# Kernel optimization log

Hardware: AMD Instinct MI355X
Metric: run time of the kernel (lower is better)

The kernel has to match this reference:

```python
import jax, jax.numpy as jnp
import numpy as np

N = 144      # Lx*Ly lattice sites (12x12)
NH = 256     # GRU hidden units
K = 2        # local Hilbert dim (occupied/empty)
LOG_EPS = 1e-10


def _gru_step(h, x, kernel, rec_kernel, bias):
    # Keras GRU cell, reset_after=True, gate order (z, r, h)
    gx = x @ kernel + bias[0]        # [B, 3*NH]
    gh = h @ rec_kernel + bias[1]    # [B, 3*NH]
    xz, xr, xh = jnp.split(gx, 3, axis=-1)
    hz, hr, hn = jnp.split(gh, 3, axis=-1)
    z = jax.nn.sigmoid(xz + hz)
    r = jax.nn.sigmoid(xr + hr)
    hh = jnp.tanh(xh + r * hn)
    return z * h + (1.0 - z) * hh


def setup_inputs() -> dict:
    key = jax.random.key(0)
    k1, k2, k3 = jax.random.split(key, 3)
    glorot = lambda k, shape: jax.random.uniform(
        k, shape, jnp.float32,
        -jnp.sqrt(6.0 / (shape[0] + shape[1])),
        jnp.sqrt(6.0 / (shape[0] + shape[1])))
    return {
        "kernel": glorot(k1, (K, 3 * NH)),
        "rec_kernel": glorot(k2, (NH, 3 * NH)),
        "bias": jnp.zeros((2, 3 * NH), jnp.float32),
        "dense_w": glorot(k3, (NH, K)),
        "dense_b": jnp.zeros((K,), jnp.float32),
        "nsamples": 1024,
    }


def reference(kernel, rec_kernel, bias, dense_w, dense_b, nsamples):
    h0 = jnp.zeros((nsamples, NH), jnp.float32)
    x0 = jnp.zeros((nsamples, K), jnp.float32)   # 0.0 * one_hot(0)
    logP0 = jnp.zeros((nsamples,), jnp.float32)
    keys = jax.random.split(jax.random.key(42), N)

    def step(carry, step_key):
        h, x, logP = carry
        h = _gru_step(h, x, kernel, rec_kernel, bias)
        probs = jax.nn.softmax(h @ dense_w + dense_b)          # [B, K]
        log_probs = jnp.log(LOG_EPS + probs)                   # matches tf.math.log(1e-10+p)
        s = jax.random.categorical(step_key, log_probs)        # [B] int
        x_new = jax.nn.one_hot(s, K, dtype=jnp.float32)
        logP = logP + jnp.take_along_axis(log_probs, s[:, None], axis=1)[:, 0]
        return (h, x_new, logP), s

    (_, _, logP), samples = jax.lax.scan(step, (h0, x0, logP0), keys)
    samples = samples.T  # [nsamples, N]
    return samples, logP
```

## Files before the change

kernel.cpp:

```cpp
#include <hip/hip_runtime.h>
#include <stdint.h>

#define N_SITES 144
#define NHID    256
#define NSAMP   1024
#define MB      4
#define TPB     768
#define PARTITIONABLE 1

__device__ __forceinline__ uint32_t rotl32(uint32_t v, uint32_t r) {
    return (v << r) | (v >> (32u - r));
}

__device__ __forceinline__ void threefry(uint32_t k0, uint32_t k1,
                                         uint32_t x0, uint32_t x1,
                                         uint32_t& o0, uint32_t& o1) {
    uint32_t ks0 = k0, ks1 = k1, ks2 = k0 ^ k1 ^ 0x1BD11BDAu;
    x0 += ks0; x1 += ks1;
#define RG4(a,b,c,d) \
    x0 += x1; x1 = rotl32(x1,a); x1 ^= x0; \
    x0 += x1; x1 = rotl32(x1,b); x1 ^= x0; \
    x0 += x1; x1 = rotl32(x1,c); x1 ^= x0; \
    x0 += x1; x1 = rotl32(x1,d); x1 ^= x0;
    RG4(13,15,26,6)  x0 += ks1; x1 += ks2 + 1u;
    RG4(17,29,16,24) x0 += ks2; x1 += ks0 + 2u;
    RG4(13,15,26,6)  x0 += ks0; x1 += ks1 + 3u;
    RG4(17,29,16,24) x0 += ks1; x1 += ks2 + 4u;
    RG4(13,15,26,6)  x0 += ks2; x1 += ks0 + 5u;
#undef RG4
    o0 = x0; o1 = x1;
}

__device__ __forceinline__ float gumbel_from_bits(uint32_t bits) {
#pragma clang fp contract(off)
    const float TINY = 1.17549435e-38f;
    uint32_t fb = (bits >> 9) | 0x3f800000u;
    float u = __uint_as_float(fb) - 1.0f;
    u = u * (1.0f - TINY) + TINY;
    u = fmaxf(TINY, u);
    return -logf(-logf(u));
}

__global__ __launch_bounds__(TPB, 1)
void rnn_sample_kernel(const float* __restrict__ kern,
                       const float* __restrict__ rec,
                       const float* __restrict__ bias,
                       const float* __restrict__ dw,
                       const float* __restrict__ db,
                       float* __restrict__ out)
{
    const int t    = threadIdx.x;
    const int blk  = blockIdx.x;
    const int b0   = blk * MB;
    const int wv   = t >> 6;
    const int lane = t & 63;

    __shared__ float4   hs4[NHID];
    __shared__ float    pacc[MB][TPB];
    __shared__ uint32_t keyA[N_SITES], keyB[N_SITES];
    __shared__ float    wred[4][8];
    __shared__ int      sPrev[MB];
    __shared__ float    lgP[MB];

    float kz0 = 0.f, kr0 = 0.f, kn0 = 0.f, kz1 = 0.f, kr1 = 0.f, kn1 = 0.f;
    float b0z = 0.f, b0r = 0.f, b0n = 0.f, b1z = 0.f, b1r = 0.f, b1n = 0.f;
    float dwa = 0.f, dwb = 0.f, dba = 0.f, dbb = 0.f;
    if (t < NHID) {
        const int c0 = t, c1 = t + 256, c2 = t + 512;
        kz0 = kern[c0];       kr0 = kern[c1];       kn0 = kern[c2];
        kz1 = kern[768 + c0]; kr1 = kern[768 + c1]; kn1 = kern[768 + c2];
        b0z = bias[c0];       b0r = bias[c1];       b0n = bias[c2];
        b1z = bias[768 + c0]; b1r = bias[768 + c1]; b1n = bias[768 + c2];
        dwa = dw[2 * t];      dwb = dw[2 * t + 1];
        dba = db[0];          dbb = db[1];
        hs4[t] = make_float4(0.f, 0.f, 0.f, 0.f);
    }
    if (t < MB) { sPrev[t] = -1; lgP[t] = 0.f; }
    if (t < N_SITES) {
        uint32_t o0, o1;
        threefry(0u, 42u, 0u, (uint32_t)t, o0, o1);
        keyA[t] = o0; keyB[t] = o1;
    }
    __syncthreads();

    for (int n = 0; n < N_SITES; ++n) {
        float a0 = 0.f, a1 = 0.f, a2 = 0.f, a3 = 0.f;
        {
            const float* rp = rec + t;
#pragma unroll 8
            for (int k = 0; k < NHID; ++k) {
                float4 h4 = hs4[k];
                float w  = rp[0];
                rp += 768;
                a0 = fmaf(h4.x, w, a0);
                a1 = fmaf(h4.y, w, a1);
                a2 = fmaf(h4.z, w, a2);
                a3 = fmaf(h4.w, w, a3);
            }
        }
        pacc[0][t] = a0; pacc[1][t] = a1; pacc[2][t] = a2; pacc[3][t] = a3;
        __syncthreads();

        float hnew[MB];
        if (t < NHID) {
            float4 ho = hs4[t];
            float hold[MB] = { ho.x, ho.y, ho.z, ho.w };
            {
#pragma clang fp contract(off)
#pragma unroll
                for (int m = 0; m < MB; ++m) {
                    const int sp = sPrev[m];
                    float xz = (sp == 0) ? kz0 : ((sp == 1) ? kz1 : 0.f);
                    float xr = (sp == 0) ? kr0 : ((sp == 1) ? kr1 : 0.f);
                    float xh = (sp == 0) ? kn0 : ((sp == 1) ? kn1 : 0.f);
                    xz = xz + b0z;  xr = xr + b0r;  xh = xh + b0n;
                    const float hz = pacc[m][t]       + b1z;
                    const float hr = pacc[m][t + 256] + b1r;
                    const float hn = pacc[m][t + 512] + b1n;
                    const float z = 1.0f / (1.0f + expf(-(xz + hz)));
                    const float r = 1.0f / (1.0f + expf(-(xr + hr)));
                    const float rhn = r * hn;
                    const float hh = tanhf(xh + rhn);
                    hnew[m] = z * hold[m] + (1.0f - z) * hh;
                }
            }
            hs4[t] = make_float4(hnew[0], hnew[1], hnew[2], hnew[3]);

#pragma unroll
            for (int m = 0; m < MB; ++m) {
                float va = hnew[m] * dwa;
                float vb = hnew[m] * dwb;
#pragma unroll
                for (int off = 32; off > 0; off >>= 1) {
                    va += __shfl_xor(va, off, 64);
                    vb += __shfl_xor(vb, off, 64);
                }
                if (lane == 0) { wred[wv][2 * m] = va; wred[wv][2 * m + 1] = vb; }
            }
        }
        __syncthreads();

        if (t < MB) {
            const int m = t;
            float l0 = wred[0][2 * m] + wred[1][2 * m] + wred[2][2 * m] + wred[3][2 * m];
            float l1 = wred[0][2 * m + 1] + wred[1][2 * m + 1] + wred[2][2 * m + 1] + wred[3][2 * m + 1];
            uint32_t o0a, o1a, o0b, o1b;
            const uint32_t fbase = 2u * (uint32_t)(b0 + m);
            threefry(keyA[n], keyB[n], 0u, fbase,      o0a, o1a);
            threefry(keyA[n], keyB[n], 0u, fbase + 1u, o0b, o1b);
            const float g0 = gumbel_from_bits(o0a ^ o1a);
            const float g1 = gumbel_from_bits(o0b ^ o1b);
            {
#pragma clang fp contract(off)
                l0 = l0 + dba;
                l1 = l1 + dbb;
                const float mx = fmaxf(l0, l1);
                const float e0 = expf(l0 - mx), e1 = expf(l1 - mx);
                const float den = e0 + e1;
                const float lp0 = logf(1e-10f + e0 / den);
                const float lp1 = logf(1e-10f + e1 / den);
                const float v0 = g0 + lp0;
                const float v1 = g1 + lp1;
                const int s = (v1 > v0) ? 1 : 0;
                sPrev[m] = s;
                lgP[m] = lgP[m] + (s ? lp1 : lp0);
                out[(size_t)(b0 + m) * N_SITES + n] = (float)s;
            }
        }
        __syncthreads();
    }

    if (t < MB) out[(size_t)NSAMP * N_SITES + (b0 + t)] = lgP[t];
}

extern "C" void kernel_launch(void* const* d_in, const int* in_sizes, int n_in,
                              void* d_out, int out_size, void* d_ws, size_t ws_size,
                              hipStream_t stream) {
    (void)in_sizes; (void)n_in; (void)d_ws; (void)ws_size; (void)out_size;
    const float* kern = (const float*)d_in[0];
    const float* rec  = (const float*)d_in[1];
    const float* bias = (const float*)d_in[2];
    const float* dwp  = (const float*)d_in[3];
    const float* dbp  = (const float*)d_in[4];
    float* out = (float*)d_out;
    rnn_sample_kernel<<<NSAMP / MB, TPB, 0, stream>>>(kern, rec, bias, dwp, dbp, out);
}
```

Before: 1.573 ms.

## Precompute Gumbel noise, spread gate math over all threads, drop per-step barrier

Before the site loop, all 144 sites' Gumbel noise is computed in parallel across threads and stored in shared memory, which takes the threefry hashing off the serial per-step sampling path. The GRU gate update, previously done by 256 threads looping over 4 samples, is now spread across all 768 threads: three samples run in parallel, then a second pass covers the fourth. The trailing __syncthreads per step is removed and logP is kept in a register. The cost is extra shared memory for the noise table and more reliance on the remaining barriers being enough to order sPrev, wred and hs4 between steps.

```diff
diff --git a/kernel.cpp b/kernel.cpp
--- a/kernel.cpp
+++ b/kernel.cpp
@@ -52,34 +52,41 @@
     const int t    = threadIdx.x;
     const int blk  = blockIdx.x;
     const int b0   = blk * MB;
-    const int wv   = t >> 6;
     const int lane = t & 63;
+    const int u    = t & 255;
+    const int m1   = t >> 8;
 
     __shared__ float4   hs4[NHID];
     __shared__ float    pacc[MB][TPB];
     __shared__ uint32_t keyA[N_SITES], keyB[N_SITES];
-    __shared__ float    wred[4][8];
+    __shared__ float    glds[N_SITES][MB][2];
+    __shared__ float    wred[MB][4][2];
     __shared__ int      sPrev[MB];
-    __shared__ float    lgP[MB];
 
-    float kz0 = 0.f, kr0 = 0.f, kn0 = 0.f, kz1 = 0.f, kr1 = 0.f, kn1 = 0.f;
-    float b0z = 0.f, b0r = 0.f, b0n = 0.f, b1z = 0.f, b1r = 0.f, b1n = 0.f;
-    float dwa = 0.f, dwb = 0.f, dba = 0.f, dbb = 0.f;
-    if (t < NHID) {
-        const int c0 = t, c1 = t + 256, c2 = t + 512;
-        kz0 = kern[c0];       kr0 = kern[c1];       kn0 = kern[c2];
-        kz1 = kern[768 + c0]; kr1 = kern[768 + c1]; kn1 = kern[768 + c2];
-        b0z = bias[c0];       b0r = bias[c1];       b0n = bias[c2];
-        b1z = bias[768 + c0]; b1r = bias[768 + c1]; b1n = bias[768 + c2];
-        dwa = dw[2 * t];      dwb = dw[2 * t + 1];
-        dba = db[0];          dbb = db[1];
-        hs4[t] = make_float4(0.f, 0.f, 0.f, 0.f);
-    }
-    if (t < MB) { sPrev[t] = -1; lgP[t] = 0.f; }
+    const float kz0 = kern[u];        const float kr0 = kern[u + 256];  const float kn0 = kern[u + 512];
+    const float kz1 = kern[768 + u];  const float kr1 = kern[768 + u + 256]; const float kn1 = kern[768 + u + 512];
+    const float b0z = bias[u];        const float b0r = bias[u + 256];  const float b0n = bias[u + 512];
+    const float b1z = bias[768 + u];  const float b1r = bias[768 + u + 256]; const float b1n = bias[768 + u + 512];
+    const float dwa = dw[2 * u];      const float dwb = dw[2 * u + 1];
+    const float dba = db[0];          const float dbb = db[1];
+    float lgPr = 0.f;
+    if (t < NHID) hs4[t] = make_float4(0.f, 0.f, 0.f, 0.f);
+    if (t < MB) sPrev[t] = -1;
     if (t < N_SITES) {
         uint32_t o0, o1;
         threefry(0u, 42u, 0u, (uint32_t)t, o0, o1);
         keyA[t] = o0; keyB[t] = o1;
+    }
+    __syncthreads();
+
+    if (t < N_SITES * MB) {
+        const int n = t >> 2, m = t & 3;
+        uint32_t o0a, o1a, o0b, o1b;
+        const uint32_t fbase = 2u * (uint32_t)(b0 + m);
+        threefry(keyA[n], keyB[n], 0u, fbase,      o0a, o1a);
+        threefry(keyA[n], keyB[n], 0u, fbase + 1u, o0b, o1b);
+        glds[n][m][0] = gumbel_from_bits(o0a ^ o1a);
+        glds[n][m][1] = gumbel_from_bits(o0b ^ o1b);
     }
     __syncthreads();
 
@@ -91,7 +98,7 @@
             for (int k = 0; k < NHID; ++k) {
                 float4 h4 = hs4[k];
                 float w  = rp[0];
-                rp += 768;
+                rp += TPB;
                 a0 = fmaf(h4.x, w, a0);
                 a1 = fmaf(h4.y, w, a1);
                 a2 = fmaf(h4.z, w, a2);
@@ -101,55 +108,46 @@
         pacc[0][t] = a0; pacc[1][t] = a1; pacc[2][t] = a2; pacc[3][t] = a3;
         __syncthreads();
 
-        float hnew[MB];
-        if (t < NHID) {
-            float4 ho = hs4[t];
-            float hold[MB] = { ho.x, ho.y, ho.z, ho.w };
+#pragma unroll
+        for (int pass = 0; pass < 2; ++pass) {
+            const int m = (pass == 0) ? m1 : 3;
+            if (pass == 1 && t >= NHID) break;
+            float hnew;
             {
 #pragma clang fp contract(off)
+                const int sp = sPrev[m];
+                float xz = (sp == 0) ? kz0 : ((sp == 1) ? kz1 : 0.f);
+                float xr = (sp == 0) ? kr0 : ((sp == 1) ? kr1 : 0.f);
+                float xh = (sp == 0) ? kn0 : ((sp == 1) ? kn1 : 0.f);
+                xz = xz + b0z;  xr = xr + b0r;  xh = xh + b0n;
+                const float hz = pacc[m][u]       + b1z;
+                const float hr = pacc[m][u + 256] + b1r;
+                const float hn = pacc[m][u + 512] + b1n;
+                const float z = 1.0f / (1.0f + expf(-(xz + hz)));
+                const float r = 1.0f / (1.0f + expf(-(xr + hr)));
+                const float rhn = r * hn;
+                const float hh = tanhf(xh + rhn);
+                const float hold = ((const float*)&hs4[u])[m];
+                hnew = z * hold + (1.0f - z) * hh;
+                ((float*)&hs4[u])[m] = hnew;
+            }
+            float va = hnew * dwa;
+            float vb = hnew * dwb;
 #pragma unroll
-                for (int m = 0; m < MB; ++m) {
-                    const int sp = sPrev[m];
-                    float xz = (sp == 0) ? kz0 : ((sp == 1) ? kz1 : 0.f);
-                    float xr = (sp == 0) ? kr0 : ((sp == 1) ? kr1 : 0.f);
-                    float xh = (sp == 0) ? kn0 : ((sp == 1) ? kn1 : 0.f);
-                    xz = xz + b0z;  xr = xr + b0r;  xh = xh + b0n;
-                    const float hz = pacc[m][t]       + b1z;
-                    const float hr = pacc[m][t + 256] + b1r;
-                    const float hn = pacc[m][t + 512] + b1n;
-                    const float z = 1.0f / (1.0f + expf(-(xz + hz)));
-                    const float r = 1.0f / (1.0f + expf(-(xr + hr)));
-                    const float rhn = r * hn;
-                    const float hh = tanhf(xh + rhn);
-                    hnew[m] = z * hold[m] + (1.0f - z) * hh;
-                }
+            for (int off = 32; off > 0; off >>= 1) {
+                va += __shfl_xor(va, off, 64);
+                vb += __shfl_xor(vb, off, 64);
             }
-            hs4[t] = make_float4(hnew[0], hnew[1], hnew[2], hnew[3]);
-
-#pragma unroll
-            for (int m = 0; m < MB; ++m) {
-                float va = hnew[m] * dwa;
-                float vb = hnew[m] * dwb;
-#pragma unroll
-                for (int off = 32; off > 0; off >>= 1) {
-                    va += __shfl_xor(va, off, 64);
-                    vb += __shfl_xor(vb, off, 64);
-                }
-                if (lane == 0) { wred[wv][2 * m] = va; wred[wv][2 * m + 1] = vb; }
-            }
+            if (lane == 0) { wred[m][u >> 6][0] = va; wred[m][u >> 6][1] = vb; }
         }
         __syncthreads();
 
         if (t < MB) {
             const int m = t;
-            float l0 = wred[0][2 * m] + wred[1][2 * m] + wred[2][2 * m] + wred[3][2 * m];
-            float l1 = wred[0][2 * m + 1] + wred[1][2 * m + 1] + wred[2][2 * m + 1] + wred[3][2 * m + 1];
-            uint32_t o0a, o1a, o0b, o1b;
-            const uint32_t fbase = 2u * (uint32_t)(b0 + m);
-            threefry(keyA[n], keyB[n], 0u, fbase,      o0a, o1a);
-            threefry(keyA[n], keyB[n], 0u, fbase + 1u, o0b, o1b);
-            const float g0 = gumbel_from_bits(o0a ^ o1a);
-            const float g1 = gumbel_from_bits(o0b ^ o1b);
+            float l0 = wred[m][0][0] + wred[m][1][0] + wred[m][2][0] + wred[m][3][0];
+            float l1 = wred[m][0][1] + wred[m][1][1] + wred[m][2][1] + wred[m][3][1];
+            const float g0 = glds[n][m][0];
+            const float g1 = glds[n][m][1];
             {
 #pragma clang fp contract(off)
                 l0 = l0 + dba;
@@ -163,14 +161,13 @@
                 const float v1 = g1 + lp1;
                 const int s = (v1 > v0) ? 1 : 0;
                 sPrev[m] = s;
-                lgP[m] = lgP[m] + (s ? lp1 : lp0);
+                lgPr = lgPr + (s ? lp1 : lp0);
                 out[(size_t)(b0 + m) * N_SITES + n] = (float)s;
             }
         }
-        __syncthreads();
     }
 
-    if (t < MB) out[(size_t)NSAMP * N_SITES + (b0 + t)] = lgP[t];
+    if (t < MB) out[(size_t)NSAMP * N_SITES + (b0 + t)] = lgPr;
 }
 
 extern "C" void kernel_launch(void* const* d_in, const int* in_sizes, int n_in,
```

Result: faster. 1.472 ms (-6.4%).
